# Optimization experiments

Hardware: AMD Instinct MI355X
Metric: run time of the kernel (lower is better)

Reference implementation:

```python
import jax, jax.numpy as jnp
import numpy as np

IOU_THRESH = 0.1
TEACHER_CONF = 0.2
EPS = 1e-7


def box_iou(box1, box2, giou=False):
    # box1: [B,m,4], box2: [B,n,4] in cxcywh -> pairwise IoU [B,m,n]
    b1 = box1[:, :, None, :]  # [B,m,1,4]
    b2 = box2[:, None, :, :]  # [B,1,n,4]
    x1, y1, w1, h1 = b1[..., 0], b1[..., 1], b1[..., 2], b1[..., 3]
    x2, y2, w2, h2 = b2[..., 0], b2[..., 1], b2[..., 2], b2[..., 3]
    b1x1, b1x2, b1y1, b1y2 = x1 - w1 / 2, x1 + w1 / 2, y1 - h1 / 2, y1 + h1 / 2
    b2x1, b2x2, b2y1, b2y2 = x2 - w2 / 2, x2 + w2 / 2, y2 - h2 / 2, y2 + h2 / 2
    inter = (jnp.maximum(jnp.minimum(b1x2, b2x2) - jnp.maximum(b1x1, b2x1), 0.0)
             * jnp.maximum(jnp.minimum(b1y2, b2y2) - jnp.maximum(b1y1, b2y1), 0.0))
    union = w1 * h1 + w2 * h2 - inter + EPS
    iou = inter / union
    if giou:
        c_area = ((jnp.maximum(b1x2, b2x2) - jnp.minimum(b1x1, b2x1))
                  * (jnp.maximum(b1y2, b2y2) - jnp.minimum(b1y1, b2y1)) + EPS)
        return iou - (c_area - union) / c_area
    return iou


def setup_inputs() -> dict:
    key = jax.random.key(0)
    k1, k2, k3, k4 = jax.random.split(key, 4)
    B, Q, C = 16, 900, 80
    return {
        "s_pred_logits": jax.random.normal(k1, (B, Q, C), dtype=jnp.float32),
        "s_pred_boxes": jax.random.uniform(k2, (B, Q, 4), dtype=jnp.float32),
        "t_pred_logits": jax.random.normal(k3, (B, Q, C), dtype=jnp.float32),
        "t_pred_boxes": jax.random.uniform(k4, (B, Q, 4), dtype=jnp.float32),
        "target_nums": 128,
    }


def reference(s_pred_logits, s_pred_boxes, t_pred_logits, t_pred_boxes, target_nums):
    B, Q, C = s_pred_logits.shape
    tn = jnp.asarray(target_nums, dtype=s_pred_logits.dtype)

    # teacher confidence flag (detached in original; bool => no grad anyway)
    conf = jax.nn.sigmoid(t_pred_logits).max(-1) > TEACHER_CONF  # [B,Q]

    # pairwise IoU and best-teacher match per student query
    iou = box_iou(s_pred_boxes, t_pred_boxes)        # [B,Q,Q]
    max_iou = iou.max(-1)                            # [B,Q]
    max_idx = jnp.argmax(iou, -1)                    # [B,Q]

    # torch: gather((max_iou>th).repeat & conf_flag, 1, idx[...,None]) reads column 0
    flag = jnp.take_along_axis(max_iou > IOU_THRESH, max_idx, axis=1) & conf[:, 0:1]  # [B,Q]

    # torch gathers column 0 of the pairwise L1 / GIoU matrices -> only t_boxes[:,0] matters
    l1_col0 = jnp.abs(s_pred_boxes - t_pred_boxes[:, 0:1, :]).sum(-1)               # [B,Q]
    giou_col0 = 1.0 - box_iou(s_pred_boxes, t_pred_boxes[:, 0:1, :], giou=True)[:, :, 0]  # [B,Q]
    l1_g = jnp.take_along_axis(l1_col0, max_idx, axis=1)
    giou_g = jnp.take_along_axis(giou_col0, max_idx, axis=1)

    lbox_l1 = jnp.where(flag, l1_g, 0.0).sum() / tn * 5.0
    lbox_iou = jnp.where(flag, giou_g, 0.0).sum() / tn * 2.0

    # pairwise BCE over flattened [B*Q] rows; torch gather picks column max_idx_flat[p]
    # (indexes rows 0..Q-1 of the flattened teacher -- faithfully reproduced)
    s_flat = s_pred_logits.reshape(B * Q, C)
    t_flat = t_pred_logits.reshape(B * Q, C)
    idx_flat = max_idx.reshape(-1)                   # values in [0,Q)
    t_probs = jax.nn.sigmoid(t_flat[idx_flat])       # [B*Q, C]
    # BCEWithLogits(x, t) = softplus(x) - x*t  (stable)
    bce = jax.nn.softplus(s_flat) - s_flat * t_probs
    lcls = bce.mean(-1).sum() / tn

    loss = lbox_l1 + lbox_iou + lcls
    return jnp.where(conf.any(), loss, 0.0)
```

## Files before the change

### kernel.cpp

```cpp
#include <hip/hip_runtime.h>
#include <math.h>

#define NB 16
#define NQ 900
#define NC 80
#define EPSV 1e-7f
#define IOU_THR 0.1f
#define SPB 16
#define CHB 57

__device__ __forceinline__ float sigm(float x) { return 1.0f / (1.0f + __expf(-x)); }

__global__ __launch_bounds__(256) void k_main(
    const float* __restrict__ s_logits,
    const float* __restrict__ s_boxes,
    const float* __restrict__ t_logits,
    const float* __restrict__ t_boxes,
    int*    __restrict__ g_cnt,
    float*  __restrict__ g_v,
    float2* __restrict__ g_part)
{
    __shared__ float4 tcor[NQ];
    __shared__ float  tarea[NQ];
    __shared__ int    lidx[SPB];
    __shared__ float  sconf0;
    __shared__ float2 sres[SPB];

    const int bx  = blockIdx.x;
    const int b   = blockIdx.y;
    const int tid = threadIdx.x;

    if (tid < SPB) sres[tid] = make_float2(0.f, 0.f);

    const float4* tb = (const float4*)(t_boxes + b * NQ * 4);
    for (int i = tid; i < NQ; i += 256) {
        float4 t = tb[i];
        float hw = t.z * 0.5f, hh = t.w * 0.5f;
        tcor[i]  = make_float4(t.x - hw, t.x + hw, t.y - hh, t.y + hh);
        tarea[i] = t.z * t.w;
    }
    if (tid < 64) {
        const float* tl = t_logits + b * NQ * NC;
        float m = tl[tid];
        if (tid < NC - 64) m = fmaxf(m, tl[tid + 64]);
        for (int s = 32; s >= 1; s >>= 1) m = fmaxf(m, __shfl_xor(m, s, 64));
        if (tid == 0) sconf0 = (sigm(m) > 0.2f) ? 1.0f : 0.0f;
    }
    __syncthreads();

    const int s  = tid >> 4;
    const int tc = tid & 15;
    const int sq = bx * SPB + s;
    const bool act = (sq < NQ);
    float best = -1.0f; int bidx = 0;
    float4 sb = make_float4(0.f, 0.f, 0.f, 0.f);
    float sx1 = 0.f, sx2 = 0.f, sy1 = 0.f, sy2 = 0.f, sarea = 0.f;
    if (act) {
        sb = ((const float4*)(s_boxes + b * NQ * 4))[sq];
        float shw = sb.z * 0.5f, shh = sb.w * 0.5f;
        sx1 = sb.x - shw; sx2 = sb.x + shw;
        sy1 = sb.y - shh; sy2 = sb.y + shh;
        sarea = sb.z * sb.w;
        #pragma unroll 4
        for (int i = 0; i < 57; ++i) {
            int t = tc + (i << 4);
            if (t < NQ) {
                float4 c = tcor[t];
                float iw = fminf(sx2, c.y) - fmaxf(sx1, c.x);
                float ih = fminf(sy2, c.w) - fmaxf(sy1, c.z);
                float inter = fmaxf(iw, 0.0f) * fmaxf(ih, 0.0f);
                float uni = sarea + tarea[t] - inter + EPSV;
                float iou = inter * __frcp_rn(uni);
                if (iou > best) { best = iou; bidx = t; }
            }
        }
    }
    for (int m = 1; m <= 8; m <<= 1) {
        float ov = __shfl_xor(best, m, 64);
        int   oi = __shfl_xor(bidx, m, 64);
        if (ov > best || (ov == best && oi < bidx)) { best = ov; bidx = oi; }
    }
    if (act && tc == 0) {
        int o = b * NQ + sq;
        lidx[s] = bidx;
        atomicAdd(&g_cnt[b * NQ + bidx], 1);
        float4 t0 = tb[0];
        float4 c  = tcor[0];
        float iw = fminf(sx2, c.y) - fmaxf(sx1, c.x);
        float ih = fminf(sy2, c.w) - fmaxf(sy1, c.z);
        float inter = fmaxf(iw, 0.0f) * fmaxf(ih, 0.0f);
        float uni = sarea + tarea[0] - inter + EPSV;
        float iou = inter / uni;
        float cw = fmaxf(sx2, c.y) - fminf(sx1, c.x);
        float ch = fmaxf(sy2, c.w) - fminf(sy1, c.z);
        float carea = cw * ch + EPSV;
        float giou1 = 1.0f - (iou - (carea - uni) / carea);
        float l1 = fabsf(sb.x - t0.x) + fabsf(sb.y - t0.y) +
                   fabsf(sb.z - t0.z) + fabsf(sb.w - t0.w);
        float v = 0.0f;
        if (sconf0 > 0.0f && best > IOU_THR) v = 5.0f * l1 + 2.0f * giou1;
        g_v[o] = v;
    }
    __syncthreads();

    const int wv  = tid >> 6, lane = tid & 63;
    const int grp = lane >> 4, tc2 = lane & 15;
    const int s2  = wv * 4 + grp;
    const int sq2 = bx * SPB + s2;
    if (sq2 < NQ) {
        int row = b * NQ + sq2;
        int j   = lidx[s2];
        const float* srow = s_logits + row * NC;
        const float* trow = t_logits + row * NC;
        const float* grow = t_logits + j * NC;
        float bce = 0.f, tmax = -1e30f;
        #pragma unroll
        for (int e = 0; e < 5; ++e) {
            int c = e * 16 + tc2;
            float s0 = srow[c], t0 = trow[c], g0 = grow[c];
            bce += fmaxf(s0, 0.f) + __logf(1.0f + __expf(-fabsf(s0)))
                 - s0 * __frcp_rn(1.0f + __expf(-g0));
            tmax = fmaxf(tmax, t0);
        }
        for (int m = 8; m >= 1; m >>= 1) {
            bce  += __shfl_xor(bce, m, 64);
            tmax  = fmaxf(tmax, __shfl_xor(tmax, m, 64));
        }
        if (tc2 == 0)
            sres[s2] = make_float2(bce * (1.0f / (float)NC),
                                   (sigm(tmax) > 0.2f) ? 1.0f : 0.0f);
    }
    __syncthreads();
    if (tid == 0) {
        float bs = 0.f, ca = 0.f;
        #pragma unroll
        for (int k = 0; k < SPB; ++k) { bs += sres[k].x; ca = fmaxf(ca, sres[k].y); }
        g_part[b * CHB + bx] = make_float2(bs, ca);
    }
}

__global__ __launch_bounds__(1024) void k_final(
    const int*    __restrict__ g_cnt,
    const float*  __restrict__ g_v,
    const float2* __restrict__ g_part,
    const int*    __restrict__ tn_p,
    float* __restrict__ out)
{
    const int tid = threadIdx.x;
    float bs = 0.f, ca = 0.f;
    if (tid < NB * CHB) { float2 p = g_part[tid]; bs = p.x; ca = p.y; }
    float vs = 0.f;
    #pragma unroll
    for (int k = 0; k < 15; ++k) {
        int i = tid + k * 1024;
        if (i < NB * NQ) vs += (float)g_cnt[i] * g_v[i];
    }
    __shared__ float rb[16], rv[16], rc[16];
    const int wv = tid >> 6, lane = tid & 63;
    for (int m = 32; m >= 1; m >>= 1) {
        bs += __shfl_xor(bs, m, 64);
        vs += __shfl_xor(vs, m, 64);
        ca  = fmaxf(ca, __shfl_xor(ca, m, 64));
    }
    if (lane == 0) { rb[wv] = bs; rv[wv] = vs; rc[wv] = ca; }
    __syncthreads();
    if (tid == 0) {
        float sb = 0.f, sv = 0.f, sc = 0.f;
        for (int k = 0; k < 16; ++k) { sb += rb[k]; sv += rv[k]; sc = fmaxf(sc, rc[k]); }
        float tn = (float)tn_p[0];
        out[0] = (sc > 0.f) ? (sv + sb) / tn : 0.0f;
    }
}

extern "C" void kernel_launch(void* const* d_in, const int* in_sizes, int n_in,
                              void* d_out, int out_size, void* d_ws, size_t ws_size,
                              hipStream_t stream) {
    const float* s_logits = (const float*)d_in[0];
    const float* s_boxes  = (const float*)d_in[1];
    const float* t_logits = (const float*)d_in[2];
    const float* t_boxes  = (const float*)d_in[3];
    const int*   tn       = (const int*)d_in[4];
    float* out = (float*)d_out;

    char* ws = (char*)d_ws;
    int*    g_cnt  = (int*)(ws);
    float*  g_v    = (float*)(ws + 57600);
    float2* g_part = (float2*)(ws + 115200);

    hipMemsetAsync(g_cnt, 0, NB * NQ * sizeof(int), stream);
    k_main<<<dim3(CHB, NB), 256, 0, stream>>>(s_logits, s_boxes, t_logits, t_boxes,
                                              g_cnt, g_v, g_part);
    k_final<<<1, 1024, 0, stream>>>(g_cnt, g_v, g_part, tn, out);
}
```

Baseline: 30.53 us.

## Process two student boxes per thread and pad teacher box table

Each thread now scores two student queries against each teacher box it reads from shared memory, doubling reuse per LDS load and halving the block count. The teacher table is padded with sentinel boxes so the inner loop drops its bounds check, and the teacher area array is replaced by recomputing the area from the corner coordinates. The block partial sum now uses a wave shuffle reduction instead of a serial loop. The shared result buffer is no longer zero-initialised, so inactive rows in the last block may contribute undefined values.

```diff
diff --git a/kernel.cpp b/kernel.cpp
--- a/kernel.cpp
+++ b/kernel.cpp
@@ -3,11 +3,12 @@
 
 #define NB 16
 #define NQ 900
+#define NQP 912
 #define NC 80
 #define EPSV 1e-7f
 #define IOU_THR 0.1f
-#define SPB 16
-#define CHB 57
+#define SPB 32
+#define CHB 29
 
 __device__ __forceinline__ float sigm(float x) { return 1.0f / (1.0f + __expf(-x)); }
 
@@ -20,8 +21,7 @@
     float*  __restrict__ g_v,
     float2* __restrict__ g_part)
 {
-    __shared__ float4 tcor[NQ];
-    __shared__ float  tarea[NQ];
+    __shared__ float4 tcor[NQP];
     __shared__ int    lidx[SPB];
     __shared__ float  sconf0;
     __shared__ float2 sres[SPB];
@@ -30,14 +30,15 @@
     const int b   = blockIdx.y;
     const int tid = threadIdx.x;
 
-    if (tid < SPB) sres[tid] = make_float2(0.f, 0.f);
-
     const float4* tb = (const float4*)(t_boxes + b * NQ * 4);
-    for (int i = tid; i < NQ; i += 256) {
-        float4 t = tb[i];
-        float hw = t.z * 0.5f, hh = t.w * 0.5f;
-        tcor[i]  = make_float4(t.x - hw, t.x + hw, t.y - hh, t.y + hh);
-        tarea[i] = t.z * t.w;
+    for (int i = tid; i < NQP; i += 256) {
+        if (i < NQ) {
+            float4 t = tb[i];
+            float hw = t.z * 0.5f, hh = t.w * 0.5f;
+            tcor[i] = make_float4(t.x - hw, t.x + hw, t.y - hh, t.y + hh);
+        } else {
+            tcor[i] = make_float4(2e9f, -2e9f, 2e9f, -2e9f);
+        }
     }
     if (tid < 64) {
         const float* tl = t_logits + b * NQ * NC;
@@ -48,94 +49,119 @@
     }
     __syncthreads();
 
-    const int s  = tid >> 4;
-    const int tc = tid & 15;
-    const int sq = bx * SPB + s;
-    const bool act = (sq < NQ);
-    float best = -1.0f; int bidx = 0;
-    float4 sb = make_float4(0.f, 0.f, 0.f, 0.f);
-    float sx1 = 0.f, sx2 = 0.f, sy1 = 0.f, sy2 = 0.f, sarea = 0.f;
-    if (act) {
-        sb = ((const float4*)(s_boxes + b * NQ * 4))[sq];
-        float shw = sb.z * 0.5f, shh = sb.w * 0.5f;
-        sx1 = sb.x - shw; sx2 = sb.x + shw;
-        sy1 = sb.y - shh; sy2 = sb.y + shh;
-        sarea = sb.z * sb.w;
-        #pragma unroll 4
-        for (int i = 0; i < 57; ++i) {
-            int t = tc + (i << 4);
-            if (t < NQ) {
-                float4 c = tcor[t];
-                float iw = fminf(sx2, c.y) - fmaxf(sx1, c.x);
-                float ih = fminf(sy2, c.w) - fmaxf(sy1, c.z);
-                float inter = fmaxf(iw, 0.0f) * fmaxf(ih, 0.0f);
-                float uni = sarea + tarea[t] - inter + EPSV;
-                float iou = inter * __frcp_rn(uni);
-                if (iou > best) { best = iou; bidx = t; }
-            }
-        }
+    const int g   = tid >> 4;
+    const int tc  = tid & 15;
+    const int sq0 = bx * SPB + g * 2;
+    const int sq1 = sq0 + 1;
+    const bool a0 = (sq0 < NQ), a1 = (sq1 < NQ);
+
+    float4 sb0 = make_float4(0.f,0.f,0.f,0.f), sb1 = sb0;
+    if (a0) sb0 = ((const float4*)(s_boxes + b * NQ * 4))[sq0];
+    if (a1) sb1 = ((const float4*)(s_boxes + b * NQ * 4))[sq1];
+    const float s0x1 = sb0.x - sb0.z*0.5f, s0x2 = sb0.x + sb0.z*0.5f;
+    const float s0y1 = sb0.y - sb0.w*0.5f, s0y2 = sb0.y + sb0.w*0.5f;
+    const float s0a  = sb0.z * sb0.w;
+    const float s1x1 = sb1.x - sb1.z*0.5f, s1x2 = sb1.x + sb1.z*0.5f;
+    const float s1y1 = sb1.y - sb1.w*0.5f, s1y2 = sb1.y + sb1.w*0.5f;
+    const float s1a  = sb1.z * sb1.w;
+
+    float best0 = -1.0f, best1 = -1.0f; int bi0 = 0, bi1 = 0;
+    #pragma unroll 4
+    for (int i = 0; i < 57; ++i) {
+        int t = tc + (i << 4);
+        float4 c = tcor[t];
+        float ta = (c.y - c.x) * (c.w - c.z);
+        float iw0 = fminf(s0x2, c.y) - fmaxf(s0x1, c.x);
+        float ih0 = fminf(s0y2, c.w) - fmaxf(s0y1, c.z);
+        float in0 = fmaxf(iw0, 0.0f) * fmaxf(ih0, 0.0f);
+        float io0 = in0 * __frcp_rn(s0a + ta - in0 + EPSV);
+        if (io0 > best0) { best0 = io0; bi0 = t; }
+        float iw1 = fminf(s1x2, c.y) - fmaxf(s1x1, c.x);
+        float ih1 = fminf(s1y2, c.w) - fmaxf(s1y1, c.z);
+        float in1 = fmaxf(iw1, 0.0f) * fmaxf(ih1, 0.0f);
+        float io1 = in1 * __frcp_rn(s1a + ta - in1 + EPSV);
+        if (io1 > best1) { best1 = io1; bi1 = t; }
     }
     for (int m = 1; m <= 8; m <<= 1) {
-        float ov = __shfl_xor(best, m, 64);
-        int   oi = __shfl_xor(bidx, m, 64);
-        if (ov > best || (ov == best && oi < bidx)) { best = ov; bidx = oi; }
-    }
-    if (act && tc == 0) {
-        int o = b * NQ + sq;
-        lidx[s] = bidx;
-        atomicAdd(&g_cnt[b * NQ + bidx], 1);
+        float ov0 = __shfl_xor(best0, m, 64); int oi0 = __shfl_xor(bi0, m, 64);
+        if (ov0 > best0 || (ov0 == best0 && oi0 < bi0)) { best0 = ov0; bi0 = oi0; }
+        float ov1 = __shfl_xor(best1, m, 64); int oi1 = __shfl_xor(bi1, m, 64);
+        if (ov1 > best1 || (ov1 == best1 && oi1 < bi1)) { best1 = ov1; bi1 = oi1; }
+    }
+    if (tc == 0) {
         float4 t0 = tb[0];
         float4 c  = tcor[0];
-        float iw = fminf(sx2, c.y) - fmaxf(sx1, c.x);
-        float ih = fminf(sy2, c.w) - fmaxf(sy1, c.z);
-        float inter = fmaxf(iw, 0.0f) * fmaxf(ih, 0.0f);
-        float uni = sarea + tarea[0] - inter + EPSV;
-        float iou = inter / uni;
-        float cw = fmaxf(sx2, c.y) - fminf(sx1, c.x);
-        float ch = fmaxf(sy2, c.w) - fminf(sy1, c.z);
-        float carea = cw * ch + EPSV;
-        float giou1 = 1.0f - (iou - (carea - uni) / carea);
-        float l1 = fabsf(sb.x - t0.x) + fabsf(sb.y - t0.y) +
-                   fabsf(sb.z - t0.z) + fabsf(sb.w - t0.w);
-        float v = 0.0f;
-        if (sconf0 > 0.0f && best > IOU_THR) v = 5.0f * l1 + 2.0f * giou1;
-        g_v[o] = v;
+        #pragma unroll
+        for (int k = 0; k < 2; ++k) {
+            const bool  ak = k ? a1 : a0;
+            if (!ak) continue;
+            const int   sq = k ? sq1 : sq0;
+            const float best = k ? best1 : best0;
+            const int   bi   = k ? bi1 : bi0;
+            const float4 sb  = k ? sb1 : sb0;
+            const float sx1 = k ? s1x1 : s0x1, sx2 = k ? s1x2 : s0x2;
+            const float sy1 = k ? s1y1 : s0y1, sy2 = k ? s1y2 : s0y2;
+            const float sa  = k ? s1a : s0a;
+            int o = b * NQ + sq;
+            lidx[g * 2 + k] = bi;
+            atomicAdd(&g_cnt[b * NQ + bi], 1);
+            float iw = fminf(sx2, c.y) - fmaxf(sx1, c.x);
+            float ih = fminf(sy2, c.w) - fmaxf(sy1, c.z);
+            float inter = fmaxf(iw, 0.0f) * fmaxf(ih, 0.0f);
+            float uni = sa + t0.z * t0.w - inter + EPSV;
+            float iou = inter / uni;
+            float cw = fmaxf(sx2, c.y) - fminf(sx1, c.x);
+            float ch = fmaxf(sy2, c.w) - fminf(sy1, c.z);
+            float carea = cw * ch + EPSV;
+            float giou1 = 1.0f - (iou - (carea - uni) / carea);
+            float l1 = fabsf(sb.x - t0.x) + fabsf(sb.y - t0.y) +
+                       fabsf(sb.z - t0.z) + fabsf(sb.w - t0.w);
+            float v = 0.0f;
+            if (sconf0 > 0.0f && best > IOU_THR) v = 5.0f * l1 + 2.0f * giou1;
+            g_v[o] = v;
+        }
     }
     __syncthreads();
 
     const int wv  = tid >> 6, lane = tid & 63;
     const int grp = lane >> 4, tc2 = lane & 15;
-    const int s2  = wv * 4 + grp;
-    const int sq2 = bx * SPB + s2;
-    if (sq2 < NQ) {
-        int row = b * NQ + sq2;
-        int j   = lidx[s2];
-        const float* srow = s_logits + row * NC;
-        const float* trow = t_logits + row * NC;
-        const float* grow = t_logits + j * NC;
-        float bce = 0.f, tmax = -1e30f;
-        #pragma unroll
-        for (int e = 0; e < 5; ++e) {
-            int c = e * 16 + tc2;
-            float s0 = srow[c], t0 = trow[c], g0 = grow[c];
-            bce += fmaxf(s0, 0.f) + __logf(1.0f + __expf(-fabsf(s0)))
-                 - s0 * __frcp_rn(1.0f + __expf(-g0));
-            tmax = fmaxf(tmax, t0);
-        }
-        for (int m = 8; m >= 1; m >>= 1) {
-            bce  += __shfl_xor(bce, m, 64);
-            tmax  = fmaxf(tmax, __shfl_xor(tmax, m, 64));
-        }
-        if (tc2 == 0)
-            sres[s2] = make_float2(bce * (1.0f / (float)NC),
-                                   (sigm(tmax) > 0.2f) ? 1.0f : 0.0f);
-    }
-    __syncthreads();
-    if (tid == 0) {
+    #pragma unroll
+    for (int pass = 0; pass < 2; ++pass) {
+        const int r   = pass * 16 + wv * 4 + grp;
+        const int sq2 = bx * SPB + r;
+        if (sq2 < NQ) {
+            int row = b * NQ + sq2;
+            int j   = lidx[r];
+            const float* srow = s_logits + row * NC;
+            const float* trow = t_logits + row * NC;
+            const float* grow = t_logits + j * NC;
+            float bce = 0.f, tmax = -1e30f;
+            #pragma unroll
+            for (int e = 0; e < 5; ++e) {
+                int cc = e * 16 + tc2;
+                float s0 = srow[cc], t0 = trow[cc], g0 = grow[cc];
+                bce += fmaxf(s0, 0.f) + __logf(1.0f + __expf(-fabsf(s0)))
+                     - s0 * __frcp_rn(1.0f + __expf(-g0));
+                tmax = fmaxf(tmax, t0);
+            }
+            for (int m = 8; m >= 1; m >>= 1) {
+                bce  += __shfl_xor(bce, m, 64);
+                tmax  = fmaxf(tmax, __shfl_xor(tmax, m, 64));
+            }
+            if (tc2 == 0)
+                sres[r] = make_float2(bce * (1.0f / (float)NC),
+                                      (sigm(tmax) > 0.2f) ? 1.0f : 0.0f);
+        }
+    }
+    __syncthreads();
+    if (tid < 64) {
         float bs = 0.f, ca = 0.f;
-        #pragma unroll
-        for (int k = 0; k < SPB; ++k) { bs += sres[k].x; ca = fmaxf(ca, sres[k].y); }
-        g_part[b * CHB + bx] = make_float2(bs, ca);
+        if (tid < SPB) { float2 p = sres[tid]; bs = p.x; ca = p.y; }
+        for (int m = 32; m >= 1; m >>= 1) {
+            bs += __shfl_xor(bs, m, 64);
+            ca  = fmaxf(ca, __shfl_xor(ca, m, 64));
+        }
+        if (tid == 0) g_part[b * CHB + bx] = make_float2(bs, ca);
     }
 }
 
```

After: 31.71 us. 3.9% more time.

## Fuse final reduction into main kernel via last-block-done atomic counter

Applied to the files above, without the earlier changes.

Removes the separate single-block final kernel. Each block now increments a global done counter, and the last block to arrive performs the global reduction and writes the loss. The BCE loads are also vectorized to float4, and the rcp uses the cheaper amdgcn builtin. This saves one kernel launch at the cost of a serialized tail reduction done by 256 threads instead of 1024.

```diff
diff --git a/kernel.cpp b/kernel.cpp
--- a/kernel.cpp
+++ b/kernel.cpp
@@ -8,6 +8,7 @@
 #define IOU_THR 0.1f
 #define SPB 16
 #define CHB 57
+#define NBLK (NB * CHB)
 
 __device__ __forceinline__ float sigm(float x) { return 1.0f / (1.0f + __expf(-x)); }
 
@@ -16,21 +17,24 @@
     const float* __restrict__ s_boxes,
     const float* __restrict__ t_logits,
     const float* __restrict__ t_boxes,
+    const int*   __restrict__ tn_p,
     int*    __restrict__ g_cnt,
+    int*    done,
     float*  __restrict__ g_v,
-    float2* __restrict__ g_part)
+    float2* __restrict__ g_part,
+    float*  __restrict__ out)
 {
     __shared__ float4 tcor[NQ];
     __shared__ float  tarea[NQ];
     __shared__ int    lidx[SPB];
     __shared__ float  sconf0;
     __shared__ float2 sres[SPB];
+    __shared__ int    winner;
+    __shared__ float  fr[12];
 
     const int bx  = blockIdx.x;
     const int b   = blockIdx.y;
     const int tid = threadIdx.x;
-
-    if (tid < SPB) sres[tid] = make_float2(0.f, 0.f);
 
     const float4* tb = (const float4*)(t_boxes + b * NQ * 4);
     for (int i = tid; i < NQ; i += 256) {
@@ -113,15 +117,24 @@
         const float* srow = s_logits + row * NC;
         const float* trow = t_logits + row * NC;
         const float* grow = t_logits + j * NC;
-        float bce = 0.f, tmax = -1e30f;
-        #pragma unroll
-        for (int e = 0; e < 5; ++e) {
-            int c = e * 16 + tc2;
-            float s0 = srow[c], t0 = trow[c], g0 = grow[c];
-            bce += fmaxf(s0, 0.f) + __logf(1.0f + __expf(-fabsf(s0)))
-                 - s0 * __frcp_rn(1.0f + __expf(-g0));
-            tmax = fmaxf(tmax, t0);
-        }
+        float4 sv = *(const float4*)(srow + tc2 * 4);
+        float4 tv = *(const float4*)(trow + tc2 * 4);
+        float4 gv = *(const float4*)(grow + tc2 * 4);
+        float  s4 = srow[64 + tc2];
+        float  t4 = trow[64 + tc2];
+        float  g4 = grow[64 + tc2];
+        float bce = 0.f;
+        {
+            float se[5] = {sv.x, sv.y, sv.z, sv.w, s4};
+            float ge[5] = {gv.x, gv.y, gv.z, gv.w, g4};
+            #pragma unroll
+            for (int e = 0; e < 5; ++e) {
+                float s0 = se[e], g0 = ge[e];
+                bce += fmaxf(s0, 0.f) + __logf(1.0f + __expf(-fabsf(s0)))
+                     - s0 * __builtin_amdgcn_rcpf(1.0f + __expf(-g0));
+            }
+        }
+        float tmax = fmaxf(fmaxf(fmaxf(tv.x, tv.y), fmaxf(tv.z, tv.w)), t4);
         for (int m = 8; m >= 1; m >>= 1) {
             bce  += __shfl_xor(bce, m, 64);
             tmax  = fmaxf(tmax, __shfl_xor(tmax, m, 64));
@@ -131,44 +144,49 @@
                                    (sigm(tmax) > 0.2f) ? 1.0f : 0.0f);
     }
     __syncthreads();
+    if (tid < 64) {
+        float bs = 0.f, ca = 0.f;
+        if (tid < SPB) { float2 p = sres[tid]; bs = p.x; ca = p.y; }
+        for (int m = 32; m >= 1; m >>= 1) {
+            bs += __shfl_xor(bs, m, 64);
+            ca  = fmaxf(ca, __shfl_xor(ca, m, 64));
+        }
+        if (tid == 0) g_part[b * CHB + bx] = make_float2(bs, ca);
+    }
+
+    __syncthreads();
     if (tid == 0) {
-        float bs = 0.f, ca = 0.f;
-        #pragma unroll
-        for (int k = 0; k < SPB; ++k) { bs += sres[k].x; ca = fmaxf(ca, sres[k].y); }
-        g_part[b * CHB + bx] = make_float2(bs, ca);
-    }
-}
-
-__global__ __launch_bounds__(1024) void k_final(
-    const int*    __restrict__ g_cnt,
-    const float*  __restrict__ g_v,
-    const float2* __restrict__ g_part,
-    const int*    __restrict__ tn_p,
-    float* __restrict__ out)
-{
-    const int tid = threadIdx.x;
-    float bs = 0.f, ca = 0.f;
-    if (tid < NB * CHB) { float2 p = g_part[tid]; bs = p.x; ca = p.y; }
-    float vs = 0.f;
-    #pragma unroll
-    for (int k = 0; k < 15; ++k) {
-        int i = tid + k * 1024;
-        if (i < NB * NQ) vs += (float)g_cnt[i] * g_v[i];
-    }
-    __shared__ float rb[16], rv[16], rc[16];
-    const int wv = tid >> 6, lane = tid & 63;
+        __threadfence();
+        int old = __hip_atomic_fetch_add(done, 1, __ATOMIC_ACQ_REL, __HIP_MEMORY_SCOPE_AGENT);
+        winner = (old == NBLK - 1) ? 1 : 0;
+    }
+    __syncthreads();
+    if (!winner) return;
+    __threadfence();
+
+    float bs = 0.f, ca = 0.f, vs = 0.f;
+    for (int i = tid; i < NBLK; i += 256) {
+        float2 p = g_part[i];
+        bs += p.x; ca = fmaxf(ca, p.y);
+    }
+    for (int i = tid; i < NB * NQ; i += 256)
+        vs += (float)g_cnt[i] * g_v[i];
     for (int m = 32; m >= 1; m >>= 1) {
         bs += __shfl_xor(bs, m, 64);
         vs += __shfl_xor(vs, m, 64);
         ca  = fmaxf(ca, __shfl_xor(ca, m, 64));
     }
-    if (lane == 0) { rb[wv] = bs; rv[wv] = vs; rc[wv] = ca; }
+    if ((tid & 63) == 0) {
+        int w = tid >> 6;
+        fr[w] = bs; fr[4 + w] = vs; fr[8 + w] = ca;
+    }
     __syncthreads();
     if (tid == 0) {
-        float sb = 0.f, sv = 0.f, sc = 0.f;
-        for (int k = 0; k < 16; ++k) { sb += rb[k]; sv += rv[k]; sc = fmaxf(sc, rc[k]); }
+        float sb2 = fr[0] + fr[1] + fr[2] + fr[3];
+        float sv2 = fr[4] + fr[5] + fr[6] + fr[7];
+        float sc2 = fmaxf(fmaxf(fr[8], fr[9]), fmaxf(fr[10], fr[11]));
         float tn = (float)tn_p[0];
-        out[0] = (sc > 0.f) ? (sv + sb) / tn : 0.0f;
+        out[0] = (sc2 > 0.f) ? (sv2 + sb2) / tn : 0.0f;
     }
 }
 
@@ -184,11 +202,11 @@
 
     char* ws = (char*)d_ws;
     int*    g_cnt  = (int*)(ws);
-    float*  g_v    = (float*)(ws + 57600);
-    float2* g_part = (float2*)(ws + 115200);
-
-    hipMemsetAsync(g_cnt, 0, NB * NQ * sizeof(int), stream);
-    k_main<<<dim3(CHB, NB), 256, 0, stream>>>(s_logits, s_boxes, t_logits, t_boxes,
-                                              g_cnt, g_v, g_part);
-    k_final<<<1, 1024, 0, stream>>>(g_cnt, g_v, g_part, tn, out);
+    int*    done   = (int*)(ws + 57600);
+    float*  g_v    = (float*)(ws + 57664);
+    float2* g_part = (float2*)(ws + 115264);
+
+    hipMemsetAsync(ws, 0, 57664, stream);
+    k_main<<<dim3(CHB, NB), 256, 0, stream>>>(s_logits, s_boxes, t_logits, t_boxes, tn,
+                                              g_cnt, done, g_v, g_part, out);
 }
```

After: 70.09 us. +129.6%, slower.

## Halve queries per block, widen IoU scan to 32 lanes with padded teacher boxes

Applied to the files above, without the earlier changes.

Each block now handles 8 student queries instead of 16, which doubles the grid to 113x16 blocks. Each query's IoU scan is split across 32 lanes over a teacher array padded to 928 entries with sentinel boxes whose IoU is zero, so the inner loop no longer needs a bounds branch. The BCE stage uses float4 vector loads and a raw reciprocal, and the per-block reduction becomes a shuffle reduction. The cost is that half the threads sit idle in the BCE stage and the per-block teacher-box staging is repeated across twice as many blocks.

```diff
diff --git a/kernel.cpp b/kernel.cpp
--- a/kernel.cpp
+++ b/kernel.cpp
@@ -3,11 +3,13 @@
 
 #define NB 16
 #define NQ 900
+#define NQP 928
 #define NC 80
 #define EPSV 1e-7f
 #define IOU_THR 0.1f
-#define SPB 16
-#define CHB 57
+#define SPB 8
+#define CHB 113
+#define NBLK (NB * CHB)
 
 __device__ __forceinline__ float sigm(float x) { return 1.0f / (1.0f + __expf(-x)); }
 
@@ -20,8 +22,8 @@
     float*  __restrict__ g_v,
     float2* __restrict__ g_part)
 {
-    __shared__ float4 tcor[NQ];
-    __shared__ float  tarea[NQ];
+    __shared__ float4 tcor[NQP];
+    __shared__ float  tarea[NQP];
     __shared__ int    lidx[SPB];
     __shared__ float  sconf0;
     __shared__ float2 sres[SPB];
@@ -33,11 +35,16 @@
     if (tid < SPB) sres[tid] = make_float2(0.f, 0.f);
 
     const float4* tb = (const float4*)(t_boxes + b * NQ * 4);
-    for (int i = tid; i < NQ; i += 256) {
-        float4 t = tb[i];
-        float hw = t.z * 0.5f, hh = t.w * 0.5f;
-        tcor[i]  = make_float4(t.x - hw, t.x + hw, t.y - hh, t.y + hh);
-        tarea[i] = t.z * t.w;
+    for (int i = tid; i < NQP; i += 256) {
+        if (i < NQ) {
+            float4 t = tb[i];
+            float hw = t.z * 0.5f, hh = t.w * 0.5f;
+            tcor[i]  = make_float4(t.x - hw, t.x + hw, t.y - hh, t.y + hh);
+            tarea[i] = t.z * t.w;
+        } else {
+            tcor[i]  = make_float4(2e9f, -2e9f, 2e9f, -2e9f);
+            tarea[i] = 1.0f;
+        }
     }
     if (tid < 64) {
         const float* tl = t_logits + b * NQ * NC;
@@ -48,8 +55,8 @@
     }
     __syncthreads();
 
-    const int s  = tid >> 4;
-    const int tc = tid & 15;
+    const int s  = tid >> 5;
+    const int tc = tid & 31;
     const int sq = bx * SPB + s;
     const bool act = (sq < NQ);
     float best = -1.0f; int bidx = 0;
@@ -62,20 +69,18 @@
         sy1 = sb.y - shh; sy2 = sb.y + shh;
         sarea = sb.z * sb.w;
         #pragma unroll 4
-        for (int i = 0; i < 57; ++i) {
-            int t = tc + (i << 4);
-            if (t < NQ) {
-                float4 c = tcor[t];
-                float iw = fminf(sx2, c.y) - fmaxf(sx1, c.x);
-                float ih = fminf(sy2, c.w) - fmaxf(sy1, c.z);
-                float inter = fmaxf(iw, 0.0f) * fmaxf(ih, 0.0f);
-                float uni = sarea + tarea[t] - inter + EPSV;
-                float iou = inter * __frcp_rn(uni);
-                if (iou > best) { best = iou; bidx = t; }
-            }
-        }
-    }
-    for (int m = 1; m <= 8; m <<= 1) {
+        for (int i = 0; i < 29; ++i) {
+            int t = tc + (i << 5);
+            float4 c = tcor[t];
+            float iw = fminf(sx2, c.y) - fmaxf(sx1, c.x);
+            float ih = fminf(sy2, c.w) - fmaxf(sy1, c.z);
+            float inter = fmaxf(iw, 0.0f) * fmaxf(ih, 0.0f);
+            float uni = sarea + tarea[t] - inter + EPSV;
+            float iou = inter * __frcp_rn(uni);
+            if (iou > best) { best = iou; bidx = t; }
+        }
+    }
+    for (int m = 1; m <= 16; m <<= 1) {
         float ov = __shfl_xor(best, m, 64);
         int   oi = __shfl_xor(bidx, m, 64);
         if (ov > best || (ov == best && oi < bidx)) { best = ov; bidx = oi; }
@@ -105,37 +110,49 @@
 
     const int wv  = tid >> 6, lane = tid & 63;
     const int grp = lane >> 4, tc2 = lane & 15;
-    const int s2  = wv * 4 + grp;
-    const int sq2 = bx * SPB + s2;
-    if (sq2 < NQ) {
+    const int r   = wv * 4 + grp;
+    const int sq2 = bx * SPB + r;
+    if (r < SPB && sq2 < NQ) {
         int row = b * NQ + sq2;
-        int j   = lidx[s2];
+        int j   = lidx[r];
         const float* srow = s_logits + row * NC;
         const float* trow = t_logits + row * NC;
         const float* grow = t_logits + j * NC;
-        float bce = 0.f, tmax = -1e30f;
-        #pragma unroll
-        for (int e = 0; e < 5; ++e) {
-            int c = e * 16 + tc2;
-            float s0 = srow[c], t0 = trow[c], g0 = grow[c];
-            bce += fmaxf(s0, 0.f) + __logf(1.0f + __expf(-fabsf(s0)))
-                 - s0 * __frcp_rn(1.0f + __expf(-g0));
-            tmax = fmaxf(tmax, t0);
-        }
+        float4 svv = *(const float4*)(srow + tc2 * 4);
+        float4 tvv = *(const float4*)(trow + tc2 * 4);
+        float4 gvv = *(const float4*)(grow + tc2 * 4);
+        float  s4 = srow[64 + tc2];
+        float  t4 = trow[64 + tc2];
+        float  g4 = grow[64 + tc2];
+        float bce = 0.f;
+        {
+            float se[5] = {svv.x, svv.y, svv.z, svv.w, s4};
+            float ge[5] = {gvv.x, gvv.y, gvv.z, gvv.w, g4};
+            #pragma unroll
+            for (int e = 0; e < 5; ++e) {
+                float s0 = se[e], g0 = ge[e];
+                bce += fmaxf(s0, 0.f) + __logf(1.0f + __expf(-fabsf(s0)))
+                     - s0 * __builtin_amdgcn_rcpf(1.0f + __expf(-g0));
+            }
+        }
+        float tmax = fmaxf(fmaxf(fmaxf(tvv.x, tvv.y), fmaxf(tvv.z, tvv.w)), t4);
         for (int m = 8; m >= 1; m >>= 1) {
             bce  += __shfl_xor(bce, m, 64);
             tmax  = fmaxf(tmax, __shfl_xor(tmax, m, 64));
         }
         if (tc2 == 0)
-            sres[s2] = make_float2(bce * (1.0f / (float)NC),
-                                   (sigm(tmax) > 0.2f) ? 1.0f : 0.0f);
-    }
-    __syncthreads();
-    if (tid == 0) {
+            sres[r] = make_float2(bce * (1.0f / (float)NC),
+                                  (sigm(tmax) > 0.2f) ? 1.0f : 0.0f);
+    }
+    __syncthreads();
+    if (tid < 64) {
         float bs = 0.f, ca = 0.f;
-        #pragma unroll
-        for (int k = 0; k < SPB; ++k) { bs += sres[k].x; ca = fmaxf(ca, sres[k].y); }
-        g_part[b * CHB + bx] = make_float2(bs, ca);
+        if (tid < SPB) { float2 p = sres[tid]; bs = p.x; ca = p.y; }
+        for (int m = 32; m >= 1; m >>= 1) {
+            bs += __shfl_xor(bs, m, 64);
+            ca  = fmaxf(ca, __shfl_xor(ca, m, 64));
+        }
+        if (tid == 0) g_part[b * CHB + bx] = make_float2(bs, ca);
     }
 }
 
@@ -148,7 +165,10 @@
 {
     const int tid = threadIdx.x;
     float bs = 0.f, ca = 0.f;
-    if (tid < NB * CHB) { float2 p = g_part[tid]; bs = p.x; ca = p.y; }
+    for (int i = tid; i < NBLK; i += 1024) {
+        float2 p = g_part[i];
+        bs += p.x; ca = fmaxf(ca, p.y);
+    }
     float vs = 0.f;
     #pragma unroll
     for (int k = 0; k < 15; ++k) {
```

After: 30.56 us. About the same (+0.1%).
